# Kernel optimization log

Hardware: AMD Instinct MI355X
Metric: run time of the kernel (lower is better)

## Reference

```python
import jax, jax.numpy as jnp
import numpy as np

N = 50000   # nodes
E = 600000  # edges
F = 128     # feat_in
H = 64      # hidden_features
H2 = 32     # hidden_features // 2


def setup_inputs() -> dict:
    key = jax.random.key(0)
    ks = jax.random.split(key, 10)
    w = lambda k, shape: jax.random.normal(k, shape, dtype=jnp.float32) * 0.05
    return {
        "x": jax.random.normal(ks[0], (N, F), dtype=jnp.float32),
        "edge_index": jax.random.randint(ks[1], (2, E), 0, N, dtype=jnp.int32),
        "edge_attr": jax.random.uniform(ks[2], (E, 1), dtype=jnp.float32),
        # GINConv 1 MLP: Linear(F,H) -> Linear(H,H), learnable eps
        "w1a": w(ks[3], (H, F)), "b1a": jnp.zeros((H,), jnp.float32),
        "w1b": w(ks[4], (H, H)), "b1b": jnp.zeros((H,), jnp.float32),
        "eps1": jnp.zeros((), jnp.float32),
        # GINConv 2 MLP: Linear(H,H2) -> Linear(H2,H2), learnable eps
        "w2a": w(ks[5], (H2, H)), "b2a": jnp.zeros((H2,), jnp.float32),
        "w2b": w(ks[6], (H2, H2)), "b2b": jnp.zeros((H2,), jnp.float32),
        "eps2": jnp.zeros((), jnp.float32),
        # SAGEConv(H2, 1): lin_l (neighbor path, has bias), lin_r (root path, no bias)
        "wl": w(ks[7], (1, H2)), "bl": jnp.zeros((1,), jnp.float32),
        "wr": w(ks[8], (1, H2)),
    }


def _gin(x, src, dst, eps, wa, ba, wb, bb):
    # GIN: MLP((1+eps)*x_i + sum_{j->i} x_j)
    agg = jax.ops.segment_sum(x[src], dst, num_segments=x.shape[0])
    h = (1.0 + eps) * x + agg
    h = h @ wa.T + ba
    return h @ wb.T + bb


def reference(x, edge_index, edge_attr, w1a, b1a, w1b, b1b, eps1,
              w2a, b2a, w2b, b2b, eps2, wl, bl, wr):
    src, dst = edge_index[0], edge_index[1]
    ew = edge_attr.squeeze()  # (E,)
    n = x.shape[0]

    h = jax.nn.relu(_gin(x, src, dst, eps1, w1a, b1a, w1b, b1b))
    # dropout is identity in eval mode
    h = jax.nn.relu(_gin(h, src, dst, eps2, w2a, b2a, w2b, b2b))

    # SAGEConv with edge weights: mean over weighted messages + root transform
    msg = ew[:, None] * h[src]                                   # (E, H2)
    num = jax.ops.segment_sum(msg, dst, num_segments=n)          # (N, H2)
    cnt = jax.ops.segment_sum(jnp.ones((msg.shape[0],), h.dtype), dst, num_segments=n)
    mean = num / jnp.maximum(cnt, 1.0)[:, None]
    out = mean @ wl.T + bl + h @ wr.T                            # (N, 1)
    return jax.nn.relu(out)
```

## Files before the change

### kernel.cpp

```cpp
#include <hip/hip_runtime.h>

#define N_NODES 50000
#define N_EDGES 600000
#define F_IN 128
#define H1 64
#define H2 32
#define NBLK ((N_NODES + 255) / 256)

__global__ __launch_bounds__(256) void prep_weights(
    const float* __restrict__ w1a, const float* __restrict__ b1a,
    const float* __restrict__ w1b, const float* __restrict__ b1b,
    const float* __restrict__ w2a, const float* __restrict__ b2a,
    const float* __restrict__ w2b, const float* __restrict__ b2b,
    float* __restrict__ M1, float* __restrict__ c1,
    float* __restrict__ M2, float* __restrict__ c2) {
  int i = blockIdx.x * 256 + threadIdx.x;
  if (i < F_IN * H1) {
    int f = i >> 6, h = i & 63;
    float s = 0.f;
    for (int m = 0; m < H1; ++m) s += w1a[m * F_IN + f] * w1b[h * H1 + m];
    M1[i] = s;
    return;
  }
  i -= F_IN * H1;
  if (i < H1) {
    float s = b1b[i];
    for (int m = 0; m < H1; ++m) s += b1a[m] * w1b[i * H1 + m];
    c1[i] = s;
    return;
  }
  i -= H1;
  if (i < H1 * H2) {
    int h = i >> 5, o = i & 31;
    float s = 0.f;
    for (int m = 0; m < H2; ++m) s += w2a[m * H1 + h] * w2b[o * H2 + m];
    M2[i] = s;
    return;
  }
  i -= H1 * H2;
  if (i < H2) {
    float s = b2b[i];
    for (int m = 0; m < H2; ++m) s += b2a[m] * w2b[i * H2 + m];
    c2[i] = s;
  }
}

__global__ __launch_bounds__(256) void count_edges(const int* __restrict__ ei,
                                                   int* __restrict__ counts) {
  int e = blockIdx.x * 256 + threadIdx.x;
  if (e >= N_EDGES) return;
  atomicAdd(&counts[ei[N_EDGES + e]], 1);
}

__global__ __launch_bounds__(256) void block_sums(const int* __restrict__ counts,
                                                  int* __restrict__ bsums) {
  __shared__ int s[256];
  int t = threadIdx.x;
  int i = blockIdx.x * 256 + t;
  s[t] = (i < N_NODES) ? counts[i] : 0;
  __syncthreads();
  for (int off = 128; off > 0; off >>= 1) {
    if (t < off) s[t] += s[t + off];
    __syncthreads();
  }
  if (t == 0) bsums[blockIdx.x] = s[0];
}

__global__ __launch_bounds__(256) void scan_bsums(const int* __restrict__ bsums,
                                                  int* __restrict__ boffs,
                                                  int* __restrict__ row_ptr) {
  __shared__ int s[256];
  int t = threadIdx.x;
  int v = (t < NBLK) ? bsums[t] : 0;
  s[t] = v;
  __syncthreads();
  for (int off = 1; off < 256; off <<= 1) {
    int u = (t >= off) ? s[t - off] : 0;
    __syncthreads();
    s[t] += u;
    __syncthreads();
  }
  if (t < NBLK) boffs[t] = s[t] - v;
  if (t == 255) row_ptr[N_NODES] = s[255];
}

__global__ __launch_bounds__(256) void emit_rowptr(const int* __restrict__ counts,
                                                   const int* __restrict__ boffs,
                                                   int* __restrict__ row_ptr,
                                                   int* __restrict__ cursor) {
  __shared__ int s[256];
  int t = threadIdx.x;
  int i = blockIdx.x * 256 + t;
  int v = (i < N_NODES) ? counts[i] : 0;
  s[t] = v;
  __syncthreads();
  for (int off = 1; off < 256; off <<= 1) {
    int u = (t >= off) ? s[t - off] : 0;
    __syncthreads();
    s[t] += u;
    __syncthreads();
  }
  if (i < N_NODES) {
    int ex = boffs[blockIdx.x] + s[t] - v;
    row_ptr[i] = ex;
    cursor[i] = ex;
  }
}

__global__ __launch_bounds__(256) void fill_csr(const int* __restrict__ ei,
                                                const float* __restrict__ ea,
                                                int* __restrict__ cursor,
                                                int* __restrict__ csr_src,
                                                float* __restrict__ csr_w) {
  int e = blockIdx.x * 256 + threadIdx.x;
  if (e >= N_EDGES) return;
  int s = ei[e];
  int d = ei[N_EDGES + e];
  int pos = atomicAdd(&cursor[d], 1);
  csr_src[pos] = s;
  csr_w[pos] = ea[e];
}

__global__ __launch_bounds__(256) void gemm1(const float* __restrict__ x,
                                             const float* __restrict__ M1,
                                             float* __restrict__ y) {
  __shared__ float sW[F_IN * H1];
  __shared__ float sX[32][H1];
  int tid = threadIdx.x;
  for (int i = tid; i < F_IN * H1; i += 256) sW[i] = M1[i];

  int row0 = blockIdx.x * 64;
  int tr = tid >> 4;
  int tc = tid & 15;
  int lrow = tid & 63;
  int kgrp = tid >> 6;
  const float* xrow = x + (long long)(row0 + lrow) * F_IN;
  bool rvalid = (row0 + lrow) < N_NODES;

  float acc[4][4] = {{0.f}};

  for (int kc = 0; kc < 4; ++kc) {
    float4 v0 = make_float4(0.f, 0.f, 0.f, 0.f);
    float4 v1 = make_float4(0.f, 0.f, 0.f, 0.f);
    if (rvalid) {
      v0 = *reinterpret_cast<const float4*>(xrow + kc * 32 + kgrp * 8);
      v1 = *reinterpret_cast<const float4*>(xrow + kc * 32 + kgrp * 8 + 4);
    }
    __syncthreads();
    sX[kgrp * 8 + 0][lrow] = v0.x;
    sX[kgrp * 8 + 1][lrow] = v0.y;
    sX[kgrp * 8 + 2][lrow] = v0.z;
    sX[kgrp * 8 + 3][lrow] = v0.w;
    sX[kgrp * 8 + 4][lrow] = v1.x;
    sX[kgrp * 8 + 5][lrow] = v1.y;
    sX[kgrp * 8 + 6][lrow] = v1.z;
    sX[kgrp * 8 + 7][lrow] = v1.w;
    __syncthreads();
#pragma unroll
    for (int k = 0; k < 32; ++k) {
      float4 a = *reinterpret_cast<const float4*>(&sX[k][tr * 4]);
      float4 b = *reinterpret_cast<const float4*>(&sW[(kc * 32 + k) * H1 + tc * 4]);
      acc[0][0] += a.x * b.x; acc[0][1] += a.x * b.y;
      acc[0][2] += a.x * b.z; acc[0][3] += a.x * b.w;
      acc[1][0] += a.y * b.x; acc[1][1] += a.y * b.y;
      acc[1][2] += a.y * b.z; acc[1][3] += a.y * b.w;
      acc[2][0] += a.z * b.x; acc[2][1] += a.z * b.y;
      acc[2][2] += a.z * b.z; acc[2][3] += a.z * b.w;
      acc[3][0] += a.w * b.x; acc[3][1] += a.w * b.y;
      acc[3][2] += a.w * b.z; acc[3][3] += a.w * b.w;
    }
  }
#pragma unroll
  for (int i = 0; i < 4; ++i) {
    int row = row0 + tr * 4 + i;
    if (row < N_NODES) {
      float4 o = make_float4(acc[i][0], acc[i][1], acc[i][2], acc[i][3]);
      *reinterpret_cast<float4*>(&y[(long long)row * H1 + tc * 4]) = o;
    }
  }
}

__global__ __launch_bounds__(256) void gin2_fused(
    const float* __restrict__ y, const int* __restrict__ row_ptr,
    const int* __restrict__ csr_src, const float* __restrict__ M2,
    const float* __restrict__ c1, const float* __restrict__ eps1p,
    float* __restrict__ z) {
  __shared__ float sM2[H1 * H2];
  __shared__ float sc1[H1];
  __shared__ float sh[4][H1];
  int tid = threadIdx.x;
  for (int i = tid; i < H1 * H2; i += 256) sM2[i] = M2[i];
  if (tid < H1) sc1[tid] = c1[tid];
  __syncthreads();
  int wave = tid >> 6, lane = tid & 63;
  int node = blockIdx.x * 4 + wave;
  float eps1 = 1.0f + *eps1p;
  float h = 0.f;
  if (node < N_NODES) {
    int start = row_ptr[node], end = row_ptr[node + 1];
    float agg = 0.f;
    int e = start;
    for (; e + 4 <= end; e += 4) {
      int s0 = csr_src[e + 0];
      int s1 = csr_src[e + 1];
      int s2 = csr_src[e + 2];
      int s3 = csr_src[e + 3];
      float a0 = y[(long long)s0 * H1 + lane];
      float a1 = y[(long long)s1 * H1 + lane];
      float a2 = y[(long long)s2 * H1 + lane];
      float a3 = y[(long long)s3 * H1 + lane];
      agg += (a0 + a1) + (a2 + a3);
    }
    float t0 = 0.f, t1 = 0.f, t2 = 0.f;
    if (e + 0 < end) t0 = y[(long long)csr_src[e + 0] * H1 + lane];
    if (e + 1 < end) t1 = y[(long long)csr_src[e + 1] * H1 + lane];
    if (e + 2 < end) t2 = y[(long long)csr_src[e + 2] * H1 + lane];
    agg += (t0 + t1) + t2;
    h = fmaxf(eps1 * y[(long long)node * H1 + lane] + agg + sc1[lane], 0.f);
  }
  sh[wave][lane] = h;
  __syncthreads();
  if (node < N_NODES) {
    int o = lane & 31, half = lane >> 5;
    float acc = 0.f;
#pragma unroll
    for (int k = 0; k < 32; ++k) {
      int kk = half * 32 + k;
      acc += sh[wave][kk] * sM2[kk * H2 + o];
    }
    acc += __shfl_xor(acc, 32);
    if (half == 0) z[(long long)node * H2 + o] = acc;
  }
}

__global__ __launch_bounds__(256) void gin3_fused(
    const float* __restrict__ z, const int* __restrict__ row_ptr,
    const int* __restrict__ csr_src, const float* __restrict__ c2,
    const float* __restrict__ eps2p, const float* __restrict__ wl,
    const float* __restrict__ wr, float* __restrict__ p,
    float* __restrict__ r) {
  int idx = blockIdx.x * 256 + threadIdx.x;
  int node = idx >> 5;
  if (node >= N_NODES) return;
  int f = idx & 31;
  int start = row_ptr[node], end = row_ptr[node + 1];
  float agg = 0.f;
  int e = start;
  for (; e + 4 <= end; e += 4) {
    int s0 = csr_src[e + 0];
    int s1 = csr_src[e + 1];
    int s2 = csr_src[e + 2];
    int s3 = csr_src[e + 3];
    float a0 = z[(long long)s0 * H2 + f];
    float a1 = z[(long long)s1 * H2 + f];
    float a2 = z[(long long)s2 * H2 + f];
    float a3 = z[(long long)s3 * H2 + f];
    agg += (a0 + a1) + (a2 + a3);
  }
  float t0 = 0.f, t1 = 0.f, t2 = 0.f;
  if (e + 0 < end) t0 = z[(long long)csr_src[e + 0] * H2 + f];
  if (e + 1 < end) t1 = z[(long long)csr_src[e + 1] * H2 + f];
  if (e + 2 < end) t2 = z[(long long)csr_src[e + 2] * H2 + f];
  agg += (t0 + t1) + t2;
  float eps2 = 1.0f + *eps2p;
  float h = fmaxf(eps2 * z[(long long)node * H2 + f] + agg + c2[f], 0.f);
  float pd = h * wl[f];
  float rd = h * wr[f];
#pragma unroll
  for (int m = 16; m >= 1; m >>= 1) {
    pd += __shfl_xor(pd, m, 32);
    rd += __shfl_xor(rd, m, 32);
  }
  if (f == 0) {
    p[node] = pd;
    r[node] = rd;
  }
}

__global__ __launch_bounds__(256) void sage_out(
    const int* __restrict__ row_ptr, const int* __restrict__ csr_src,
    const float* __restrict__ csr_w, const float* __restrict__ p,
    const float* __restrict__ r, const float* __restrict__ blp,
    float* __restrict__ out) {
  int idx = blockIdx.x * 256 + threadIdx.x;
  int node = idx >> 4;
  if (node >= N_NODES) return;
  int l = idx & 15;
  int start = row_ptr[node], end = row_ptr[node + 1];
  float acc = 0.f;
  for (int e = start + l; e < end; e += 16) acc += csr_w[e] * p[csr_src[e]];
#pragma unroll
  for (int m = 8; m >= 1; m >>= 1) acc += __shfl_xor(acc, m, 16);
  if (l == 0) {
    float mean = acc / fmaxf((float)(end - start), 1.0f);
    out[node] = fmaxf(mean + blp[0] + r[node], 0.f);
  }
}

extern "C" void kernel_launch(void* const* d_in, const int* in_sizes, int n_in,
                              void* d_out, int out_size, void* d_ws,
                              size_t ws_size, hipStream_t stream) {
  const float* x = (const float*)d_in[0];
  const int* ei = (const int*)d_in[1];
  const float* ea = (const float*)d_in[2];
  const float* w1a = (const float*)d_in[3];
  const float* b1a = (const float*)d_in[4];
  const float* w1b = (const float*)d_in[5];
  const float* b1b = (const float*)d_in[6];
  const float* eps1 = (const float*)d_in[7];
  const float* w2a = (const float*)d_in[8];
  const float* b2a = (const float*)d_in[9];
  const float* w2b = (const float*)d_in[10];
  const float* b2b = (const float*)d_in[11];
  const float* eps2 = (const float*)d_in[12];
  const float* wl = (const float*)d_in[13];
  const float* bl = (const float*)d_in[14];
  const float* wr = (const float*)d_in[15];
  float* out = (float*)d_out;

  float* ws = (float*)d_ws;
  float* M1 = ws;
  float* c1 = M1 + F_IN * H1;
  float* M2 = c1 + H1;
  float* c2 = M2 + H1 * H2;
  float* y = c2 + H2;
  float* z = y + (long long)N_NODES * H1;
  float* p = z + (long long)N_NODES * H2;
  float* r = p + N_NODES;
  float* csr_w = r + N_NODES;
  int* counts = (int*)(csr_w + N_EDGES);
  int* cursor = counts + N_NODES;
  int* row_ptr = cursor + N_NODES;
  int* csr_src = row_ptr + N_NODES + 1;
  int* bsums = csr_src + N_EDGES;
  int* boffs = bsums + NBLK;

  hipMemsetAsync(counts, 0, sizeof(int) * (size_t)N_NODES, stream);

  prep_weights<<<41, 256, 0, stream>>>(w1a, b1a, w1b, b1b, w2a, b2a, w2b, b2b,
                                       M1, c1, M2, c2);

  count_edges<<<(N_EDGES + 255) / 256, 256, 0, stream>>>(ei, counts);
  block_sums<<<NBLK, 256, 0, stream>>>(counts, bsums);
  scan_bsums<<<1, 256, 0, stream>>>(bsums, boffs, row_ptr);
  emit_rowptr<<<NBLK, 256, 0, stream>>>(counts, boffs, row_ptr, cursor);
  fill_csr<<<(N_EDGES + 255) / 256, 256, 0, stream>>>(ei, ea, cursor, csr_src,
                                                      csr_w);

  gemm1<<<(N_NODES + 63) / 64, 256, 0, stream>>>(x, M1, y);

  gin2_fused<<<(N_NODES + 3) / 4, 256, 0, stream>>>(y, row_ptr, csr_src, M2,
                                                    c1, eps1, z);

  gin3_fused<<<(N_NODES * 32 + 255) / 256, 256, 0, stream>>>(
      z, row_ptr, csr_src, c2, eps2, wl, wr, p, r);

  sage_out<<<(N_NODES * 16 + 255) / 256, 256, 0, stream>>>(row_ptr, csr_src,
                                                           csr_w, p, r, bl, out);
}
```

Measured before the change: 250.3 us.

## Store intermediate features in bf16, interleave CSR, split gin2 into gather and GEMM

Intermediate node features y and z are stored as packed bf16 pairs, halving the bytes read by the random neighbour gathers. The CSR source and weight arrays are interleaved into one int2 array. The edge-count pass is merged into the weight-prep kernel with vectorized loads. The fused gin2 kernel is split into a gather kernel that writes fp32 h and a separate tiled GEMM, so each step can use more parallelism. This adds a kernel launch and an extra fp32 round trip for h, and the bf16 rounding reduces accuracy.

```diff
diff --git a/kernel.cpp b/kernel.cpp
--- a/kernel.cpp
+++ b/kernel.cpp
@@ -6,14 +6,40 @@
 #define H1 64
 #define H2 32
 #define NBLK ((N_NODES + 255) / 256)
-
-__global__ __launch_bounds__(256) void prep_weights(
+#define PREP_BLOCKS 41
+#define CNT_BLOCKS ((N_EDGES / 4 + 255) / 256)
+
+__device__ inline unsigned bf_round(float x) {
+  unsigned u = __float_as_uint(x);
+  u += 0x7FFFu + ((u >> 16) & 1u);
+  return u >> 16;
+}
+__device__ inline unsigned pack_bf2(float a, float b) {
+  return (bf_round(b) << 16) | bf_round(a);
+}
+__device__ inline float2 unpack_bf2(unsigned u) {
+  return make_float2(__uint_as_float(u << 16), __uint_as_float(u & 0xFFFF0000u));
+}
+
+__global__ __launch_bounds__(256) void prep_and_count(
     const float* __restrict__ w1a, const float* __restrict__ b1a,
     const float* __restrict__ w1b, const float* __restrict__ b1b,
     const float* __restrict__ w2a, const float* __restrict__ b2a,
     const float* __restrict__ w2b, const float* __restrict__ b2b,
     float* __restrict__ M1, float* __restrict__ c1,
-    float* __restrict__ M2, float* __restrict__ c2) {
+    float* __restrict__ M2, float* __restrict__ c2,
+    const int* __restrict__ ei, int* __restrict__ counts) {
+  if (blockIdx.x >= PREP_BLOCKS) {
+    int t = (blockIdx.x - PREP_BLOCKS) * 256 + threadIdx.x;
+    if (t < N_EDGES / 4) {
+      int4 d4 = *reinterpret_cast<const int4*>(&ei[N_EDGES + t * 4]);
+      atomicAdd(&counts[d4.x], 1);
+      atomicAdd(&counts[d4.y], 1);
+      atomicAdd(&counts[d4.z], 1);
+      atomicAdd(&counts[d4.w], 1);
+    }
+    return;
+  }
   int i = blockIdx.x * 256 + threadIdx.x;
   if (i < F_IN * H1) {
     int f = i >> 6, h = i & 63;
@@ -43,13 +69,6 @@
     for (int m = 0; m < H2; ++m) s += b2a[m] * w2b[i * H2 + m];
     c2[i] = s;
   }
-}
-
-__global__ __launch_bounds__(256) void count_edges(const int* __restrict__ ei,
-                                                   int* __restrict__ counts) {
-  int e = blockIdx.x * 256 + threadIdx.x;
-  if (e >= N_EDGES) return;
-  atomicAdd(&counts[ei[N_EDGES + e]], 1);
 }
 
 __global__ __launch_bounds__(256) void block_sums(const int* __restrict__ counts,
@@ -110,20 +129,18 @@
 __global__ __launch_bounds__(256) void fill_csr(const int* __restrict__ ei,
                                                 const float* __restrict__ ea,
                                                 int* __restrict__ cursor,
-                                                int* __restrict__ csr_src,
-                                                float* __restrict__ csr_w) {
+                                                int2* __restrict__ csr) {
   int e = blockIdx.x * 256 + threadIdx.x;
   if (e >= N_EDGES) return;
   int s = ei[e];
   int d = ei[N_EDGES + e];
   int pos = atomicAdd(&cursor[d], 1);
-  csr_src[pos] = s;
-  csr_w[pos] = ea[e];
+  csr[pos] = make_int2(s, __float_as_int(ea[e]));
 }
 
 __global__ __launch_bounds__(256) void gemm1(const float* __restrict__ x,
                                              const float* __restrict__ M1,
-                                             float* __restrict__ y) {
+                                             unsigned* __restrict__ ybf) {
   __shared__ float sW[F_IN * H1];
   __shared__ float sX[32][H1];
   int tid = threadIdx.x;
@@ -174,121 +191,165 @@
   for (int i = 0; i < 4; ++i) {
     int row = row0 + tr * 4 + i;
     if (row < N_NODES) {
-      float4 o = make_float4(acc[i][0], acc[i][1], acc[i][2], acc[i][3]);
-      *reinterpret_cast<float4*>(&y[(long long)row * H1 + tc * 4]) = o;
+      uint2 o;
+      o.x = pack_bf2(acc[i][0], acc[i][1]);
+      o.y = pack_bf2(acc[i][2], acc[i][3]);
+      *reinterpret_cast<uint2*>(&ybf[(long long)row * 32 + tc * 2]) = o;
     }
   }
 }
 
-__global__ __launch_bounds__(256) void gin2_fused(
-    const float* __restrict__ y, const int* __restrict__ row_ptr,
-    const int* __restrict__ csr_src, const float* __restrict__ M2,
-    const float* __restrict__ c1, const float* __restrict__ eps1p,
-    float* __restrict__ z) {
-  __shared__ float sM2[H1 * H2];
-  __shared__ float sc1[H1];
-  __shared__ float sh[4][H1];
+__global__ __launch_bounds__(256) void agg_h(
+    const unsigned* __restrict__ ybf, const int* __restrict__ row_ptr,
+    const int2* __restrict__ csr, const float* __restrict__ c1,
+    const float* __restrict__ eps1p, float* __restrict__ h) {
   int tid = threadIdx.x;
-  for (int i = tid; i < H1 * H2; i += 256) sM2[i] = M2[i];
-  if (tid < H1) sc1[tid] = c1[tid];
+  int node = blockIdx.x * 8 + (tid >> 5);
+  if (node >= N_NODES) return;
+  int j = tid & 31;
+  int start = row_ptr[node], end = row_ptr[node + 1];
+  float a0 = 0.f, a1 = 0.f;
+  int e = start;
+  for (; e + 4 <= end; e += 4) {
+    int s0 = csr[e + 0].x;
+    int s1 = csr[e + 1].x;
+    int s2 = csr[e + 2].x;
+    int s3 = csr[e + 3].x;
+    float2 u0 = unpack_bf2(ybf[(unsigned)s0 * 32 + j]);
+    float2 u1 = unpack_bf2(ybf[(unsigned)s1 * 32 + j]);
+    float2 u2 = unpack_bf2(ybf[(unsigned)s2 * 32 + j]);
+    float2 u3 = unpack_bf2(ybf[(unsigned)s3 * 32 + j]);
+    a0 += (u0.x + u1.x) + (u2.x + u3.x);
+    a1 += (u0.y + u1.y) + (u2.y + u3.y);
+  }
+  float2 t0 = make_float2(0.f, 0.f), t1 = make_float2(0.f, 0.f),
+         t2 = make_float2(0.f, 0.f);
+  if (e + 0 < end) t0 = unpack_bf2(ybf[(unsigned)csr[e + 0].x * 32 + j]);
+  if (e + 1 < end) t1 = unpack_bf2(ybf[(unsigned)csr[e + 1].x * 32 + j]);
+  if (e + 2 < end) t2 = unpack_bf2(ybf[(unsigned)csr[e + 2].x * 32 + j]);
+  a0 += (t0.x + t1.x) + t2.x;
+  a1 += (t0.y + t1.y) + t2.y;
+  float eps1 = 1.0f + *eps1p;
+  float2 self = unpack_bf2(ybf[(unsigned)node * 32 + j]);
+  float2 c = *reinterpret_cast<const float2*>(&c1[2 * j]);
+  float2 hv;
+  hv.x = fmaxf(eps1 * self.x + a0 + c.x, 0.f);
+  hv.y = fmaxf(eps1 * self.y + a1 + c.y, 0.f);
+  *reinterpret_cast<float2*>(&h[(long long)node * H1 + 2 * j]) = hv;
+}
+
+__global__ __launch_bounds__(256) void gemm2(const float* __restrict__ h,
+                                             const float* __restrict__ M2,
+                                             unsigned* __restrict__ zbf) {
+  __shared__ float sW[H1 * H2];
+  __shared__ float sX[H1][64];
+  int tid = threadIdx.x;
+  for (int i = tid; i < H1 * H2; i += 256) sW[i] = M2[i];
+
+  int row0 = blockIdx.x * 64;
+  int lrow = tid & 63;
+  int kg = tid >> 6;
+  bool rv = (row0 + lrow) < N_NODES;
+  float4 v[4] = {};
+  if (rv) {
+    const float* hr = h + (long long)(row0 + lrow) * H1 + kg * 16;
+#pragma unroll
+    for (int q = 0; q < 4; ++q) v[q] = *reinterpret_cast<const float4*>(hr + q * 4);
+  }
+#pragma unroll
+  for (int q = 0; q < 4; ++q) {
+    sX[kg * 16 + q * 4 + 0][lrow] = v[q].x;
+    sX[kg * 16 + q * 4 + 1][lrow] = v[q].y;
+    sX[kg * 16 + q * 4 + 2][lrow] = v[q].z;
+    sX[kg * 16 + q * 4 + 3][lrow] = v[q].w;
+  }
   __syncthreads();
-  int wave = tid >> 6, lane = tid & 63;
-  int node = blockIdx.x * 4 + wave;
-  float eps1 = 1.0f + *eps1p;
-  float h = 0.f;
-  if (node < N_NODES) {
-    int start = row_ptr[node], end = row_ptr[node + 1];
-    float agg = 0.f;
-    int e = start;
-    for (; e + 4 <= end; e += 4) {
-      int s0 = csr_src[e + 0];
-      int s1 = csr_src[e + 1];
-      int s2 = csr_src[e + 2];
-      int s3 = csr_src[e + 3];
-      float a0 = y[(long long)s0 * H1 + lane];
-      float a1 = y[(long long)s1 * H1 + lane];
-      float a2 = y[(long long)s2 * H1 + lane];
-      float a3 = y[(long long)s3 * H1 + lane];
-      agg += (a0 + a1) + (a2 + a3);
-    }
-    float t0 = 0.f, t1 = 0.f, t2 = 0.f;
-    if (e + 0 < end) t0 = y[(long long)csr_src[e + 0] * H1 + lane];
-    if (e + 1 < end) t1 = y[(long long)csr_src[e + 1] * H1 + lane];
-    if (e + 2 < end) t2 = y[(long long)csr_src[e + 2] * H1 + lane];
-    agg += (t0 + t1) + t2;
-    h = fmaxf(eps1 * y[(long long)node * H1 + lane] + agg + sc1[lane], 0.f);
-  }
-  sh[wave][lane] = h;
-  __syncthreads();
-  if (node < N_NODES) {
-    int o = lane & 31, half = lane >> 5;
-    float acc = 0.f;
-#pragma unroll
-    for (int k = 0; k < 32; ++k) {
-      int kk = half * 32 + k;
-      acc += sh[wave][kk] * sM2[kk * H2 + o];
-    }
-    acc += __shfl_xor(acc, 32);
-    if (half == 0) z[(long long)node * H2 + o] = acc;
-  }
-}
-
-__global__ __launch_bounds__(256) void gin3_fused(
-    const float* __restrict__ z, const int* __restrict__ row_ptr,
-    const int* __restrict__ csr_src, const float* __restrict__ c2,
+  int tr = tid >> 4;
+  int tc = tid & 15;
+  float acc[4][2] = {{0.f}};
+#pragma unroll
+  for (int k = 0; k < H1; ++k) {
+    float4 a = *reinterpret_cast<const float4*>(&sX[k][tr * 4]);
+    float2 b = *reinterpret_cast<const float2*>(&sW[k * H2 + tc * 2]);
+    acc[0][0] += a.x * b.x; acc[0][1] += a.x * b.y;
+    acc[1][0] += a.y * b.x; acc[1][1] += a.y * b.y;
+    acc[2][0] += a.z * b.x; acc[2][1] += a.z * b.y;
+    acc[3][0] += a.w * b.x; acc[3][1] += a.w * b.y;
+  }
+#pragma unroll
+  for (int i = 0; i < 4; ++i) {
+    int row = row0 + tr * 4 + i;
+    if (row < N_NODES)
+      zbf[(long long)row * 16 + tc] = pack_bf2(acc[i][0], acc[i][1]);
+  }
+}
+
+__global__ __launch_bounds__(256) void gin3(
+    const unsigned* __restrict__ zbf, const int* __restrict__ row_ptr,
+    const int2* __restrict__ csr, const float* __restrict__ c2,
     const float* __restrict__ eps2p, const float* __restrict__ wl,
     const float* __restrict__ wr, float* __restrict__ p,
     float* __restrict__ r) {
-  int idx = blockIdx.x * 256 + threadIdx.x;
-  int node = idx >> 5;
+  int tid = blockIdx.x * 256 + threadIdx.x;
+  int node = tid >> 4;
   if (node >= N_NODES) return;
-  int f = idx & 31;
+  int j = tid & 15;
   int start = row_ptr[node], end = row_ptr[node + 1];
-  float agg = 0.f;
+  float a0 = 0.f, a1 = 0.f;
   int e = start;
   for (; e + 4 <= end; e += 4) {
-    int s0 = csr_src[e + 0];
-    int s1 = csr_src[e + 1];
-    int s2 = csr_src[e + 2];
-    int s3 = csr_src[e + 3];
-    float a0 = z[(long long)s0 * H2 + f];
-    float a1 = z[(long long)s1 * H2 + f];
-    float a2 = z[(long long)s2 * H2 + f];
-    float a3 = z[(long long)s3 * H2 + f];
-    agg += (a0 + a1) + (a2 + a3);
-  }
-  float t0 = 0.f, t1 = 0.f, t2 = 0.f;
-  if (e + 0 < end) t0 = z[(long long)csr_src[e + 0] * H2 + f];
-  if (e + 1 < end) t1 = z[(long long)csr_src[e + 1] * H2 + f];
-  if (e + 2 < end) t2 = z[(long long)csr_src[e + 2] * H2 + f];
-  agg += (t0 + t1) + t2;
+    int s0 = csr[e + 0].x;
+    int s1 = csr[e + 1].x;
+    int s2 = csr[e + 2].x;
+    int s3 = csr[e + 3].x;
+    float2 u0 = unpack_bf2(zbf[(unsigned)s0 * 16 + j]);
+    float2 u1 = unpack_bf2(zbf[(unsigned)s1 * 16 + j]);
+    float2 u2 = unpack_bf2(zbf[(unsigned)s2 * 16 + j]);
+    float2 u3 = unpack_bf2(zbf[(unsigned)s3 * 16 + j]);
+    a0 += (u0.x + u1.x) + (u2.x + u3.x);
+    a1 += (u0.y + u1.y) + (u2.y + u3.y);
+  }
+  float2 t0 = make_float2(0.f, 0.f), t1 = make_float2(0.f, 0.f),
+         t2 = make_float2(0.f, 0.f);
+  if (e + 0 < end) t0 = unpack_bf2(zbf[(unsigned)csr[e + 0].x * 16 + j]);
+  if (e + 1 < end) t1 = unpack_bf2(zbf[(unsigned)csr[e + 1].x * 16 + j]);
+  if (e + 2 < end) t2 = unpack_bf2(zbf[(unsigned)csr[e + 2].x * 16 + j]);
+  a0 += (t0.x + t1.x) + t2.x;
+  a1 += (t0.y + t1.y) + t2.y;
   float eps2 = 1.0f + *eps2p;
-  float h = fmaxf(eps2 * z[(long long)node * H2 + f] + agg + c2[f], 0.f);
-  float pd = h * wl[f];
-  float rd = h * wr[f];
-#pragma unroll
-  for (int m = 16; m >= 1; m >>= 1) {
-    pd += __shfl_xor(pd, m, 32);
-    rd += __shfl_xor(rd, m, 32);
-  }
-  if (f == 0) {
+  float2 self = unpack_bf2(zbf[(unsigned)node * 16 + j]);
+  float2 c = *reinterpret_cast<const float2*>(&c2[2 * j]);
+  float h0 = fmaxf(eps2 * self.x + a0 + c.x, 0.f);
+  float h1 = fmaxf(eps2 * self.y + a1 + c.y, 0.f);
+  float2 l = *reinterpret_cast<const float2*>(&wl[2 * j]);
+  float2 w = *reinterpret_cast<const float2*>(&wr[2 * j]);
+  float pd = h0 * l.x + h1 * l.y;
+  float rd = h0 * w.x + h1 * w.y;
+#pragma unroll
+  for (int m = 8; m >= 1; m >>= 1) {
+    pd += __shfl_xor(pd, m, 16);
+    rd += __shfl_xor(rd, m, 16);
+  }
+  if (j == 0) {
     p[node] = pd;
     r[node] = rd;
   }
 }
 
 __global__ __launch_bounds__(256) void sage_out(
-    const int* __restrict__ row_ptr, const int* __restrict__ csr_src,
-    const float* __restrict__ csr_w, const float* __restrict__ p,
-    const float* __restrict__ r, const float* __restrict__ blp,
-    float* __restrict__ out) {
+    const int* __restrict__ row_ptr, const int2* __restrict__ csr,
+    const float* __restrict__ p, const float* __restrict__ r,
+    const float* __restrict__ blp, float* __restrict__ out) {
   int idx = blockIdx.x * 256 + threadIdx.x;
   int node = idx >> 4;
   if (node >= N_NODES) return;
   int l = idx & 15;
   int start = row_ptr[node], end = row_ptr[node + 1];
   float acc = 0.f;
-  for (int e = start + l; e < end; e += 16) acc += csr_w[e] * p[csr_src[e]];
+  for (int e = start + l; e < end; e += 16) {
+    int2 c = csr[e];
+    acc += __int_as_float(c.y) * p[c.x];
+  }
 #pragma unroll
   for (int m = 8; m >= 1; m >>= 1) acc += __shfl_xor(acc, m, 16);
   if (l == 0) {
@@ -323,38 +384,37 @@
   float* c1 = M1 + F_IN * H1;
   float* M2 = c1 + H1;
   float* c2 = M2 + H1 * H2;
-  float* y = c2 + H2;
-  float* z = y + (long long)N_NODES * H1;
-  float* p = z + (long long)N_NODES * H2;
+  unsigned* ybf = (unsigned*)(c2 + H2);
+  float* h = (float*)(ybf + (size_t)N_NODES * 32);
+  unsigned* zbf = (unsigned*)(h + (size_t)N_NODES * H1);
+  float* p = (float*)(zbf + (size_t)N_NODES * 16);
   float* r = p + N_NODES;
-  float* csr_w = r + N_NODES;
-  int* counts = (int*)(csr_w + N_EDGES);
+  int2* csr = (int2*)(r + N_NODES);
+  int* counts = (int*)(csr + N_EDGES);
   int* cursor = counts + N_NODES;
-  int* row_ptr = cursor + N_NODES;
-  int* csr_src = row_ptr + N_NODES + 1;
-  int* bsums = csr_src + N_EDGES;
+  int* bsums = cursor + N_NODES;
   int* boffs = bsums + NBLK;
+  int* row_ptr = boffs + NBLK;
 
   hipMemsetAsync(counts, 0, sizeof(int) * (size_t)N_NODES, stream);
 
-  prep_weights<<<41, 256, 0, stream>>>(w1a, b1a, w1b, b1b, w2a, b2a, w2b, b2b,
-                                       M1, c1, M2, c2);
-
-  count_edges<<<(N_EDGES + 255) / 256, 256, 0, stream>>>(ei, counts);
+  prep_and_count<<<PREP_BLOCKS + CNT_BLOCKS, 256, 0, stream>>>(
+      w1a, b1a, w1b, b1b, w2a, b2a, w2b, b2b, M1, c1, M2, c2, ei, counts);
+
   block_sums<<<NBLK, 256, 0, stream>>>(counts, bsums);
   scan_bsums<<<1, 256, 0, stream>>>(bsums, boffs, row_ptr);
   emit_rowptr<<<NBLK, 256, 0, stream>>>(counts, boffs, row_ptr, cursor);
-  fill_csr<<<(N_EDGES + 255) / 256, 256, 0, stream>>>(ei, ea, cursor, csr_src,
-                                                      csr_w);
-
-  gemm1<<<(N_NODES + 63) / 64, 256, 0, stream>>>(x, M1, y);
-
-  gin2_fused<<<(N_NODES + 3) / 4, 256, 0, stream>>>(y, row_ptr, csr_src, M2,
-                                                    c1, eps1, z);
-
-  gin3_fused<<<(N_NODES * 32 + 255) / 256, 256, 0, stream>>>(
-      z, row_ptr, csr_src, c2, eps2, wl, wr, p, r);
-
-  sage_out<<<(N_NODES * 16 + 255) / 256, 256, 0, stream>>>(row_ptr, csr_src,
-                                                           csr_w, p, r, bl, out);
-}
+  fill_csr<<<(N_EDGES + 255) / 256, 256, 0, stream>>>(ei, ea, cursor, csr);
+
+  gemm1<<<(N_NODES + 63) / 64, 256, 0, stream>>>(x, M1, ybf);
+
+  agg_h<<<(N_NODES + 7) / 8, 256, 0, stream>>>(ybf, row_ptr, csr, c1, eps1, h);
+
+  gemm2<<<(N_NODES + 63) / 64, 256, 0, stream>>>(h, M2, zbf);
+
+  gin3<<<(N_NODES * 16 + 255) / 256, 256, 0, stream>>>(zbf, row_ptr, csr, c2,
+                                                       eps2, wl, wr, p, r);
+
+  sage_out<<<(N_NODES * 16 + 255) / 256, 256, 0, stream>>>(row_ptr, csr, p, r,
+                                                           bl, out);
+}
```

New measurement: 240.1 us. 4.1% less time.
